# Performance work log

Measured on AMD Instinct MI355X. Metric: run time of the kernel, lower is better.

## Reference

```python
import jax, jax.numpy as jnp
import numpy as np

R = 64          # n_rois
B = 128         # batch_size (graphs)
IN = 2048       # voxels per ROI
HID = 512       # max(32, IN//4)
ROI_OUT = 20
G1, G2 = 64, 128
FC1, FC2, OUT = 512, 1024, 6400
N = R * B       # total graph nodes


def _block_complete_edges():
    # per-sample complete directed graph over R ROIs (no self loops)
    r = np.arange(R)
    s, d = np.meshgrid(r, r, indexing='ij')
    m = s != d
    s, d = s[m], d[m]                       # [R*(R-1)]
    off = (np.arange(B) * R)[:, None]       # [B,1]
    src = (s[None, :] + off).reshape(-1)
    dst = (d[None, :] + off).reshape(-1)
    return np.stack([src, dst]).astype(np.int64)  # [2, E]


def setup_inputs() -> dict:
    key = jax.random.key(0)
    ks = jax.random.split(key, 16)
    sd = lambda *s: 1.0 / np.sqrt(s[0])
    inp = {
        'x': jax.random.normal(ks[0], (R, B * IN), jnp.float32),
        'edge_index': jnp.asarray(_block_complete_edges()),
        'batch': jnp.repeat(jnp.arange(B, dtype=jnp.int64), R),
        # per-ROI MLP params (batched over ROI axis)
        'W1': jax.random.normal(ks[1], (R, IN, HID), jnp.float32) * sd(IN),
        'b1': jnp.zeros((R, HID), jnp.float32),
        'W2': jax.random.normal(ks[2], (R, HID, ROI_OUT), jnp.float32) * sd(HID),
        'b2': jnp.zeros((R, ROI_OUT), jnp.float32),
        # GCN params
        'Wg1': jax.random.normal(ks[3], (ROI_OUT, G1), jnp.float32) * sd(ROI_OUT),
        'bg1': jnp.zeros((G1,), jnp.float32),
        'Wg2': jax.random.normal(ks[4], (G1, G2), jnp.float32) * sd(G1),
        'bg2': jnp.zeros((G2,), jnp.float32),
        # FC stack
        'Wf1': jax.random.normal(ks[5], (G2, FC1), jnp.float32) * sd(G2),
        'bf1': jnp.zeros((FC1,), jnp.float32),
        'Wf2': jax.random.normal(ks[6], (FC1, FC2), jnp.float32) * sd(FC1),
        'bf2': jnp.zeros((FC2,), jnp.float32),
        'Wo': jax.random.normal(ks[7], (FC2, OUT), jnp.float32) * sd(FC2),
        'bo': jnp.zeros((OUT,), jnp.float32),
    }
    return inp


def _gcn(h, src, dst, W, b):
    # PyG GCNConv: symmetric norm with self loops, then linear
    loop = jnp.arange(N)
    s = jnp.concatenate([src, loop])
    d = jnp.concatenate([dst, loop])
    deg = jax.ops.segment_sum(jnp.ones(s.shape[0], h.dtype), d, num_segments=N)
    dinv = jax.lax.rsqrt(deg)  # deg >= 1 due to self loops
    hw = h @ W                                  # [N, out]
    msg = hw[s] * (dinv[s] * dinv[d])[:, None]  # [E+N, out]
    return jax.ops.segment_sum(msg, d, num_segments=N) + b


def reference(x, edge_index, batch, W1, b1, W2, b2, Wg1, bg1, Wg2, bg2,
              Wf1, bf1, Wf2, bf2, Wo, bo):
    # per-ROI MLPs, batched: x[r] holds B contiguous chunks of IN voxels
    xr = x.reshape(R, B, IN)
    h = jax.nn.relu(jnp.einsum('rbi,rih->rbh', xr, W1) + b1[:, None, :])
    f = jnp.einsum('rbh,rho->rbo', h, W2) + b2[:, None, :]   # [R,B,ROI_OUT]
    # node order in torch code: for b: for r -> node = b*R + r
    node_feats = f.transpose(1, 0, 2).reshape(N, ROI_OUT)

    src, dst = edge_index[0], edge_index[1]
    g = jax.nn.relu(_gcn(node_feats, src, dst, Wg1, bg1))
    g = jax.nn.relu(_gcn(g, src, dst, Wg2, bg2))

    # global mean pool over each graph's R nodes
    pooled = jax.ops.segment_sum(g, batch, num_segments=B) / R  # [B, G2]

    y = jax.nn.relu(pooled @ Wf1 + bf1)
    y = jax.nn.relu(y @ Wf2 + bf2)
    return y @ Wo + bo  # [B, OUT]
```

## Files before the change

### kernel.cpp

```cpp
#include <hip/hip_runtime.h>
#include <hip/hip_bf16.h>
#include <cstdint>

typedef float  f32x4 __attribute__((ext_vector_type(4)));
typedef short  s16x4 __attribute__((ext_vector_type(4)));
typedef short  s16x8 __attribute__((ext_vector_type(8)));
typedef __bf16 bf16x8 __attribute__((ext_vector_type(8)));
typedef unsigned int u32x2 __attribute__((ext_vector_type(2)));
typedef unsigned int u32x4 __attribute__((ext_vector_type(4)));

static __device__ __forceinline__ unsigned short f2bf(float f) {
  union { float f; unsigned u; } v; v.f = f;
  unsigned r = v.u + 0x7fffu + ((v.u >> 16) & 1u);
  return (unsigned short)(r >> 16);
}

static __device__ __forceinline__ unsigned pk2(float lo, float hi) {
  unsigned r;
  asm("v_cvt_pk_bf16_f32 %0, %1, %2" : "=v"(r) : "v"(lo), "v"(hi));
  return r;
}

static __device__ __forceinline__ f32x4 mfma16(bf16x8 a, bf16x8 b, f32x4 c) {
  return __builtin_amdgcn_mfma_f32_16x16x32_bf16(a, b, c, 0, 0, 0);
}

__global__ __launch_bounds__(256)
void k_mlp(const float* __restrict__ X, const float* __restrict__ W1,
           const float* __restrict__ b1, const float* __restrict__ W2,
           float* __restrict__ m1)
{
  __shared__ short lds_a[128 * 72];
  __shared__ short lds_b[64 * 72];
  __shared__ short lds_h[128 * 72];
  __shared__ short lds_w2[32 * 72];
  __shared__ float biasS[64];

  const int bid = blockIdx.x;
  const int r = (bid & 7) + ((bid >> 6) << 3);
  const int c = (bid >> 3) & 7;

  const float* xr = X + (long)r * (128 * 2048);
  const float* wr = W1 + (long)r * (2048 * 512) + c * 64;
  const float* bp = b1 + (long)r * 512 + c * 64;

  const int t = threadIdx.x;
  const int lane = t & 63;
  const int w = t >> 6;

  if (t < 64) biasS[t] = bp[t];

  const int aRow = t >> 2;
  const int aCol = (t & 3) * 4;
  const int bn   = t & 63;
  const int bk0  = w * 8;

  f32x4 aR[2][4];
  float bR[2][8];

  auto loadTile = [&](int ks) {
    const float* xp = xr + (long)aRow * 2048 + ks * 64 + aCol;
#pragma unroll
    for (int j = 0; j < 4; j++) {
      aR[0][j] = *(const f32x4*)(xp + 16 * j);
      aR[1][j] = *(const f32x4*)(xp + 64 * 2048 + 16 * j);
    }
    const float* wp = wr + (long)(ks * 64 + bk0) * 512 + bn;
#pragma unroll
    for (int g = 0; g < 2; g++)
#pragma unroll
      for (int j = 0; j < 8; j++)
        bR[g][j] = wp[(long)(g * 32 + j) * 512];
  };

  auto storeTile = [&]() {
#pragma unroll
    for (int g = 0; g < 2; g++)
#pragma unroll
      for (int j = 0; j < 4; j++) {
        u32x2 v;
        v[0] = pk2(aR[g][j][0], aR[g][j][1]);
        v[1] = pk2(aR[g][j][2], aR[g][j][3]);
        *(u32x2*)&lds_a[(aRow + 64 * g) * 72 + aCol + 16 * j] = v;
      }
#pragma unroll
    for (int g = 0; g < 2; g++) {
      u32x4 v;
      v[0] = pk2(bR[g][0], bR[g][1]);
      v[1] = pk2(bR[g][2], bR[g][3]);
      v[2] = pk2(bR[g][4], bR[g][5]);
      v[3] = pk2(bR[g][6], bR[g][7]);
      *(u32x4*)&lds_b[bn * 72 + bk0 + g * 32] = v;
    }
  };

  const int wm = w & 1, wn = w >> 1;
  const int mBase = wm * 64, nBase = wn * 32;
  const int lm = lane & 15, lg = lane >> 4;

  f32x4 acc[4][2];
#pragma unroll
  for (int i = 0; i < 4; i++)
#pragma unroll
    for (int j = 0; j < 2; j++) acc[i][j] = f32x4{0.f, 0.f, 0.f, 0.f};

  loadTile(0);
  for (int ks = 0; ks < 32; ks++) {
    __syncthreads();
    storeTile();
    __syncthreads();
    if (ks + 1 < 32) loadTile(ks + 1);
    bf16x8 af[2][4], bfr[2][2];
#pragma unroll
    for (int g = 0; g < 2; g++) {
#pragma unroll
      for (int i = 0; i < 4; i++)
        af[g][i] = *(const bf16x8*)&lds_a[(mBase + i * 16 + lm) * 72 + g * 32 + lg * 8];
#pragma unroll
      for (int j = 0; j < 2; j++)
        bfr[g][j] = *(const bf16x8*)&lds_b[(nBase + j * 16 + lm) * 72 + g * 32 + lg * 8];
    }
#pragma unroll
    for (int mi = 0; mi < 4; mi++)
#pragma unroll
      for (int ni = 0; ni < 2; ni++) {
        acc[mi][ni] = mfma16(af[0][mi], bfr[0][ni], acc[mi][ni]);
        acc[mi][ni] = mfma16(af[1][mi], bfr[1][ni], acc[mi][ni]);
      }
  }

#pragma unroll
  for (int mi = 0; mi < 4; mi++)
#pragma unroll
    for (int ni = 0; ni < 2; ni++) {
      const int col = nBase + ni * 16 + lm;
      const float bv = biasS[col];
#pragma unroll
      for (int i = 0; i < 4; i++) {
        const int row = mBase + mi * 16 + lg * 4 + i;
        float v = acc[mi][ni][i] + bv;
        v = v > 0.f ? v : 0.f;
        lds_h[row * 72 + col] = (short)f2bf(v);
      }
    }
  {
    const float* w2r = W2 + (long)r * (512 * 20) + (long)c * 64 * 20;
#pragma unroll
    for (int i = 0; i < 8; i++) {
      const int idx = t * 8 + i;
      const int o = idx >> 6, kh = idx & 63;
      const float v = (o < 20) ? w2r[(long)kh * 20 + o] : 0.f;
      lds_w2[o * 72 + kh] = (short)f2bf(v);
    }
  }
  __syncthreads();
  f32x4 acc2[2][2];
#pragma unroll
  for (int i = 0; i < 2; i++)
#pragma unroll
    for (int j = 0; j < 2; j++) acc2[i][j] = f32x4{0.f, 0.f, 0.f, 0.f};
#pragma unroll
  for (int ks2 = 0; ks2 < 2; ks2++) {
    bf16x8 a0 = *(const bf16x8*)&lds_h[(w * 32 + lm) * 72 + ks2 * 32 + lg * 8];
    bf16x8 a1 = *(const bf16x8*)&lds_h[(w * 32 + 16 + lm) * 72 + ks2 * 32 + lg * 8];
    bf16x8 b0 = *(const bf16x8*)&lds_w2[lm * 72 + ks2 * 32 + lg * 8];
    bf16x8 b1v = *(const bf16x8*)&lds_w2[(16 + lm) * 72 + ks2 * 32 + lg * 8];
    acc2[0][0] = mfma16(a0, b0, acc2[0][0]);
    acc2[0][1] = mfma16(a0, b1v, acc2[0][1]);
    acc2[1][0] = mfma16(a1, b0, acc2[1][0]);
    acc2[1][1] = mfma16(a1, b1v, acc2[1][1]);
  }
#pragma unroll
  for (int mi = 0; mi < 2; mi++)
#pragma unroll
    for (int ni = 0; ni < 2; ni++)
#pragma unroll
      for (int i = 0; i < 4; i++) {
        const int m = w * 32 + mi * 16 + lg * 4 + i;
        const int o = ni * 16 + lm;
        if (o < 20)
          atomicAdd(&m1[m * 20 + o], acc2[mi][ni][i] * (1.f / 64.f));
      }
}

template<int RELU>
__global__ __launch_bounds__(256)
void gemm_n64(const float* __restrict__ X, int ldx,
              const float* __restrict__ W, int ldw,
              const float* __restrict__ bias,
              float* __restrict__ out, int ldo, int kSteps)
{
  __shared__ short lds_a[128 * 72];
  __shared__ short lds_b[64 * 72];
  __shared__ float biasS[64];

  const int c = blockIdx.x;
  const int t = threadIdx.x;
  const int lane = t & 63;
  const int w = t >> 6;

  if (t < 64) biasS[t] = bias[c * 64 + t];

  const int aRow = t >> 2;
  const int aCol = (t & 3) * 4;
  const int bn   = t & 63;
  const int bk0  = w * 8;

  f32x4 aR[2][4];
  float bR[2][8];

  auto loadTile = [&](int ks) {
    const float* xp = X + (long)aRow * ldx + ks * 64 + aCol;
#pragma unroll
    for (int j = 0; j < 4; j++) {
      aR[0][j] = *(const f32x4*)(xp + 16 * j);
      aR[1][j] = *(const f32x4*)(xp + (long)64 * ldx + 16 * j);
    }
    const float* wp = W + (long)(ks * 64 + bk0) * ldw + c * 64 + bn;
#pragma unroll
    for (int g = 0; g < 2; g++)
#pragma unroll
      for (int j = 0; j < 8; j++)
        bR[g][j] = wp[(long)(g * 32 + j) * ldw];
  };

  auto storeTile = [&]() {
#pragma unroll
    for (int g = 0; g < 2; g++)
#pragma unroll
      for (int j = 0; j < 4; j++) {
        u32x2 v;
        v[0] = pk2(aR[g][j][0], aR[g][j][1]);
        v[1] = pk2(aR[g][j][2], aR[g][j][3]);
        *(u32x2*)&lds_a[(aRow + 64 * g) * 72 + aCol + 16 * j] = v;
      }
#pragma unroll
    for (int g = 0; g < 2; g++) {
      u32x4 v;
      v[0] = pk2(bR[g][0], bR[g][1]);
      v[1] = pk2(bR[g][2], bR[g][3]);
      v[2] = pk2(bR[g][4], bR[g][5]);
      v[3] = pk2(bR[g][6], bR[g][7]);
      *(u32x4*)&lds_b[bn * 72 + bk0 + g * 32] = v;
    }
  };

  const int wm = w & 1, wn = w >> 1;
  const int mBase = wm * 64, nBase = wn * 32;
  const int lm = lane & 15, lg = lane >> 4;

  f32x4 acc[4][2];
#pragma unroll
  for (int i = 0; i < 4; i++)
#pragma unroll
    for (int j = 0; j < 2; j++) acc[i][j] = f32x4{0.f, 0.f, 0.f, 0.f};

  loadTile(0);
  for (int ks = 0; ks < kSteps; ks++) {
    __syncthreads();
    storeTile();
    __syncthreads();
    if (ks + 1 < kSteps) loadTile(ks + 1);
    bf16x8 af[2][4], bfr[2][2];
#pragma unroll
    for (int g = 0; g < 2; g++) {
#pragma unroll
      for (int i = 0; i < 4; i++)
        af[g][i] = *(const bf16x8*)&lds_a[(mBase + i * 16 + lm) * 72 + g * 32 + lg * 8];
#pragma unroll
      for (int j = 0; j < 2; j++)
        bfr[g][j] = *(const bf16x8*)&lds_b[(nBase + j * 16 + lm) * 72 + g * 32 + lg * 8];
    }
#pragma unroll
    for (int mi = 0; mi < 4; mi++)
#pragma unroll
      for (int ni = 0; ni < 2; ni++) {
        acc[mi][ni] = mfma16(af[0][mi], bfr[0][ni], acc[mi][ni]);
        acc[mi][ni] = mfma16(af[1][mi], bfr[1][ni], acc[mi][ni]);
      }
  }

  float* outp = out + c * 64;
#pragma unroll
  for (int mi = 0; mi < 4; mi++)
#pragma unroll
    for (int ni = 0; ni < 2; ni++) {
      const int col = nBase + ni * 16 + lm;
      const float bv = biasS[col];
#pragma unroll
      for (int i = 0; i < 4; i++) {
        const int row = mBase + mi * 16 + lg * 4 + i;
        float v = acc[mi][ni][i] + bv;
        if (RELU) v = v > 0.f ? v : 0.f;
        outp[(long)row * ldo + col] = v;
      }
    }
}

__global__ void k_init_m1(const float* __restrict__ b2, float* __restrict__ m1) {
  const int i = blockIdx.x * blockDim.x + threadIdx.x;
  if (i >= 128 * 20) return;
  const int o = i % 20;
  float s = 0.f;
  for (int r = 0; r < 64; r++) s += b2[r * 20 + o];
  m1[i] = s * (1.f / 64.f);
}

template<int K, int RELU>
__global__ void k_fc_small(const float* __restrict__ in, const float* __restrict__ Wt,
                           const float* __restrict__ bias, float* __restrict__ out,
                           int N)
{
  const int i = blockIdx.x * blockDim.x + threadIdx.x;
  const int b = i / N;
  if (b >= 128) return;
  const int j = i - b * N;
  float s = bias[j];
  const float* ip = in + (long)b * K;
#pragma unroll
  for (int k = 0; k < K; k++) s += ip[k] * Wt[k * N + j];
  out[i] = (RELU && s < 0.f) ? 0.f : s;
}

extern "C" void kernel_launch(void* const* d_in, const int* in_sizes, int n_in,
                              void* d_out, int out_size, void* d_ws, size_t ws_size,
                              hipStream_t stream)
{
  const float* x   = (const float*)d_in[0];
  const float* W1  = (const float*)d_in[3];
  const float* b1  = (const float*)d_in[4];
  const float* W2  = (const float*)d_in[5];
  const float* b2  = (const float*)d_in[6];
  const float* Wg1 = (const float*)d_in[7];
  const float* bg1 = (const float*)d_in[8];
  const float* Wg2 = (const float*)d_in[9];
  const float* bg2 = (const float*)d_in[10];
  const float* Wf1 = (const float*)d_in[11];
  const float* bf1 = (const float*)d_in[12];
  const float* Wf2 = (const float*)d_in[13];
  const float* bf2 = (const float*)d_in[14];
  const float* Wo  = (const float*)d_in[15];
  const float* bo  = (const float*)d_in[16];
  float* out = (float*)d_out;

  float* ws = (float*)d_ws;
  float* m1 = ws;
  float* g1 = ws + 4096;
  float* g2 = ws + 16384;
  float* y1 = ws + 32768;
  float* y2 = ws + 98304;

  k_init_m1<<<10, 256, 0, stream>>>(b2, m1);
  k_mlp<<<512, 256, 0, stream>>>(x, W1, b1, W2, m1);
  k_fc_small<20, 1><<<32, 256, 0, stream>>>(m1, Wg1, bg1, g1, 64);
  k_fc_small<64, 1><<<64, 256, 0, stream>>>(g1, Wg2, bg2, g2, 128);
  gemm_n64<1><<<8,   256, 0, stream>>>(g2, 128,  Wf1, 512,  bf1, y1, 512, 2);
  gemm_n64<1><<<16,  256, 0, stream>>>(y1, 512,  Wf2, 1024, bf2, y2, 1024, 8);
  gemm_n64<0><<<100, 256, 0, stream>>>(y2, 1024, Wo,  6400, bo,  out, 6400, 16);
}
```

Baseline: 504.7 us.

## Widen per-ROI MLP block tile to 128 hidden columns with 512 threads

Each k_mlp block now covers 128 hidden units instead of 64. It uses 512 threads in 8 waves and launches half as many blocks. The point is to halve how often each ROI's X slab is re-read across the column blocks, and to halve the atomic reductions into m1. The cost is more LDS per block (a wider h tile and W2 tile), a single resident block per CU at this grid size, and less load issued per thread for the A tile.

After: 498.1 us. No clear change (-1.3%).

```diff
diff --git a/kernel.cpp b/kernel.cpp
--- a/kernel.cpp
+++ b/kernel.cpp
@@ -25,46 +25,44 @@
   return __builtin_amdgcn_mfma_f32_16x16x32_bf16(a, b, c, 0, 0, 0);
 }
 
-__global__ __launch_bounds__(256)
+__global__ __launch_bounds__(512)
 void k_mlp(const float* __restrict__ X, const float* __restrict__ W1,
            const float* __restrict__ b1, const float* __restrict__ W2,
            float* __restrict__ m1)
 {
   __shared__ short lds_a[128 * 72];
-  __shared__ short lds_b[64 * 72];
-  __shared__ short lds_h[128 * 72];
-  __shared__ short lds_w2[32 * 72];
-  __shared__ float biasS[64];
+  __shared__ short lds_b[128 * 72];
+  __shared__ short lds_h[128 * 136];
+  __shared__ short lds_w2[32 * 136];
+  __shared__ float biasS[128];
 
   const int bid = blockIdx.x;
-  const int r = (bid & 7) + ((bid >> 6) << 3);
-  const int c = (bid >> 3) & 7;
+  const int r = (bid & 7) + ((bid >> 5) << 3);
+  const int c = (bid >> 3) & 3;
 
   const float* xr = X + (long)r * (128 * 2048);
-  const float* wr = W1 + (long)r * (2048 * 512) + c * 64;
-  const float* bp = b1 + (long)r * 512 + c * 64;
+  const float* wr = W1 + (long)r * (2048 * 512) + c * 128;
+  const float* bp = b1 + (long)r * 512 + c * 128;
 
   const int t = threadIdx.x;
   const int lane = t & 63;
   const int w = t >> 6;
 
-  if (t < 64) biasS[t] = bp[t];
+  if (t < 128) biasS[t] = bp[t];
 
   const int aRow = t >> 2;
   const int aCol = (t & 3) * 4;
-  const int bn   = t & 63;
-  const int bk0  = w * 8;
-
-  f32x4 aR[2][4];
+  const int bn   = t & 127;
+  const int bk0  = (t >> 7) * 8;
+
+  f32x4 aR[4];
   float bR[2][8];
 
   auto loadTile = [&](int ks) {
     const float* xp = xr + (long)aRow * 2048 + ks * 64 + aCol;
 #pragma unroll
-    for (int j = 0; j < 4; j++) {
-      aR[0][j] = *(const f32x4*)(xp + 16 * j);
-      aR[1][j] = *(const f32x4*)(xp + 64 * 2048 + 16 * j);
-    }
+    for (int j = 0; j < 4; j++)
+      aR[j] = *(const f32x4*)(xp + 16 * j);
     const float* wp = wr + (long)(ks * 64 + bk0) * 512 + bn;
 #pragma unroll
     for (int g = 0; g < 2; g++)
@@ -75,14 +73,12 @@
 
   auto storeTile = [&]() {
 #pragma unroll
-    for (int g = 0; g < 2; g++)
-#pragma unroll
-      for (int j = 0; j < 4; j++) {
-        u32x2 v;
-        v[0] = pk2(aR[g][j][0], aR[g][j][1]);
-        v[1] = pk2(aR[g][j][2], aR[g][j][3]);
-        *(u32x2*)&lds_a[(aRow + 64 * g) * 72 + aCol + 16 * j] = v;
-      }
+    for (int j = 0; j < 4; j++) {
+      u32x2 v;
+      v[0] = pk2(aR[j][0], aR[j][1]);
+      v[1] = pk2(aR[j][2], aR[j][3]);
+      *(u32x2*)&lds_a[aRow * 72 + aCol + 16 * j] = v;
+    }
 #pragma unroll
     for (int g = 0; g < 2; g++) {
       u32x4 v;
@@ -140,47 +136,40 @@
         const int row = mBase + mi * 16 + lg * 4 + i;
         float v = acc[mi][ni][i] + bv;
         v = v > 0.f ? v : 0.f;
-        lds_h[row * 72 + col] = (short)f2bf(v);
+        lds_h[row * 136 + col] = (short)f2bf(v);
       }
     }
   {
-    const float* w2r = W2 + (long)r * (512 * 20) + (long)c * 64 * 20;
+    const float* w2r = W2 + (long)r * (512 * 20) + (long)(c * 128) * 20;
 #pragma unroll
     for (int i = 0; i < 8; i++) {
       const int idx = t * 8 + i;
-      const int o = idx >> 6, kh = idx & 63;
+      const int o = idx >> 7, kh = idx & 127;
       const float v = (o < 20) ? w2r[(long)kh * 20 + o] : 0.f;
-      lds_w2[o * 72 + kh] = (short)f2bf(v);
+      lds_w2[o * 136 + kh] = (short)f2bf(v);
     }
   }
   __syncthreads();
-  f32x4 acc2[2][2];
-#pragma unroll
-  for (int i = 0; i < 2; i++)
-#pragma unroll
-    for (int j = 0; j < 2; j++) acc2[i][j] = f32x4{0.f, 0.f, 0.f, 0.f};
-#pragma unroll
-  for (int ks2 = 0; ks2 < 2; ks2++) {
-    bf16x8 a0 = *(const bf16x8*)&lds_h[(w * 32 + lm) * 72 + ks2 * 32 + lg * 8];
-    bf16x8 a1 = *(const bf16x8*)&lds_h[(w * 32 + 16 + lm) * 72 + ks2 * 32 + lg * 8];
-    bf16x8 b0 = *(const bf16x8*)&lds_w2[lm * 72 + ks2 * 32 + lg * 8];
-    bf16x8 b1v = *(const bf16x8*)&lds_w2[(16 + lm) * 72 + ks2 * 32 + lg * 8];
-    acc2[0][0] = mfma16(a0, b0, acc2[0][0]);
-    acc2[0][1] = mfma16(a0, b1v, acc2[0][1]);
-    acc2[1][0] = mfma16(a1, b0, acc2[1][0]);
-    acc2[1][1] = mfma16(a1, b1v, acc2[1][1]);
+  f32x4 acc2[2];
+  acc2[0] = f32x4{0.f, 0.f, 0.f, 0.f};
+  acc2[1] = f32x4{0.f, 0.f, 0.f, 0.f};
+#pragma unroll
+  for (int ks2 = 0; ks2 < 4; ks2++) {
+    bf16x8 a0 = *(const bf16x8*)&lds_h[(w * 16 + lm) * 136 + ks2 * 32 + lg * 8];
+    bf16x8 b0 = *(const bf16x8*)&lds_w2[lm * 136 + ks2 * 32 + lg * 8];
+    bf16x8 b1v = *(const bf16x8*)&lds_w2[(16 + lm) * 136 + ks2 * 32 + lg * 8];
+    acc2[0] = mfma16(a0, b0, acc2[0]);
+    acc2[1] = mfma16(a0, b1v, acc2[1]);
   }
 #pragma unroll
-  for (int mi = 0; mi < 2; mi++)
-#pragma unroll
-    for (int ni = 0; ni < 2; ni++)
-#pragma unroll
-      for (int i = 0; i < 4; i++) {
-        const int m = w * 32 + mi * 16 + lg * 4 + i;
-        const int o = ni * 16 + lm;
-        if (o < 20)
-          atomicAdd(&m1[m * 20 + o], acc2[mi][ni][i] * (1.f / 64.f));
-      }
+  for (int ni = 0; ni < 2; ni++)
+#pragma unroll
+    for (int i = 0; i < 4; i++) {
+      const int m = w * 16 + lg * 4 + i;
+      const int o = ni * 16 + lm;
+      if (o < 20)
+        atomicAdd(&m1[m * 20 + o], acc2[ni][i] * (1.f / 64.f));
+    }
 }
 
 template<int RELU>
@@ -351,7 +340,7 @@
   float* y2 = ws + 98304;
 
   k_init_m1<<<10, 256, 0, stream>>>(b2, m1);
-  k_mlp<<<512, 256, 0, stream>>>(x, W1, b1, W2, m1);
+  k_mlp<<<256, 512, 0, stream>>>(x, W1, b1, W2, m1);
   k_fc_small<20, 1><<<32, 256, 0, stream>>>(m1, Wg1, bg1, g1, 64);
   k_fc_small<64, 1><<<64, 256, 0, stream>>>(g1, Wg2, bg2, g2, 128);
   gemm_n64<1><<<8,   256, 0, stream>>>(g2, 128,  Wf1, 512,  bf1, y1, 512, 2);
```
